# Kernel tuning notes

Measured on AMD Instinct MI355X. Metric: run time of the kernel, lower is better.

## Reference

```python
import jax, jax.numpy as jnp
import numpy as np

N = 50000        # nodes
E = 800000       # edges (pre self-loops)
H = 1            # heads
D = 64           # out_channels (incl. Lorentz time coord)
IN = 128         # in_channels
C = 1.0          # curvature c (Lorentz k)
EPS = 1e-6
NEG = 0.2        # leaky_relu negative slope


def segment_softmax(logits, seg, n):
    # numerically stable softmax over edges grouped by destination node
    m = jax.ops.segment_max(logits, seg, num_segments=n)
    m = jnp.where(jnp.isfinite(m), m, 0.0)
    e = jnp.exp(logits - m[seg])
    s = jax.ops.segment_sum(e, seg, num_segments=n)
    return e / (s[seg] + 1e-16)


def setup_inputs() -> dict:
    key = jax.random.key(0)
    k1, k2, k3, k4, k5 = jax.random.split(key, 5)
    x = jax.random.normal(k1, (N, IN), jnp.float32)
    fan = IN + H * (D - 1)
    W = jax.random.uniform(k2, (IN, H * (D - 1)), jnp.float32, -1.0, 1.0) * (6.0 / fan) ** 0.5
    b = jnp.zeros((H * (D - 1),), jnp.float32)
    att = jax.random.uniform(k3, (1, H, 2 * D), jnp.float32, -1.0, 1.0) * (6.0 / (H + 2 * D)) ** 0.5
    # random edges with no self loops (module removes them then re-adds canonical loops)
    src = jax.random.randint(k4, (E,), 0, N, jnp.int32)
    off = jax.random.randint(k5, (E,), 1, N, jnp.int32)
    dst = (src + off) % N
    edge_index = jnp.stack([src, dst], axis=0)
    return {"x": x, "W": W, "b": b, "att": att, "edge_index": edge_index}


def reference(x, W, b, att, edge_index):
    sqrt_c = C ** 0.5
    # add self loops
    loops = jnp.arange(N, dtype=edge_index.dtype)
    ei = jnp.concatenate([edge_index, jnp.stack([loops, loops])], axis=1)
    i, j = ei[0], ei[1]

    # hy_linear (plain Linear on Lorentz branch), then project to hyperboloid
    xs = (x @ W + b).reshape(N, H, D - 1)                       # space coords
    t = jnp.sqrt(jnp.sum(xs * xs, -1, keepdims=True) + C)       # time coord
    ox = jnp.concatenate([t, xs], -1)                           # (N,H,D) on manifold

    # Lorentz logmap0: d0 * (0, xs/||xs||), d0 = sqrt(c)*arccosh(x0/sqrt(c))
    nrm = jnp.sqrt(jnp.sum(xs * xs, -1, keepdims=True) + 1e-15)
    d0 = sqrt_c * jnp.arccosh(jnp.maximum(t / sqrt_c, 1.0 + EPS))
    log_x = jnp.concatenate([jnp.zeros_like(t), d0 * xs / nrm], -1)  # (N,H,D)

    x_i, x_j = log_x[i], log_x[j]        # (E2,H,D) edge gathers
    ox_i, ox_j = ox[i], ox[j]

    # attention logits
    alpha = jnp.sum(jnp.concatenate([x_i, x_j], -1) * att, -1)  # (E2,H)

    # distance-aware weighting: sqdist = c * arccosh(-<x,y>_L / c)^2
    inner = -ox_i[..., 0] * ox_j[..., 0] + jnp.sum(ox_i[..., 1:] * ox_j[..., 1:], -1)
    sqd = C * jnp.arccosh(jnp.maximum(-inner / C, 1.0 + EPS)) ** 2
    alpha = alpha * segment_softmax(sqd, i, N)

    alpha = jnp.where(alpha >= 0, alpha, NEG * alpha)           # leaky_relu
    alpha = segment_softmax(alpha, i, N)                        # (E2,H)

    out = jax.ops.segment_sum(alpha[..., None] * x_j, i, num_segments=N)  # (N,H,D)

    # proj_tan0 -> act -> proj_tan0
    out = out.at[..., 0].set(0.0)
    out = jax.nn.relu(out)
    out = out.at[..., 0].set(0.0)

    # expmap0 then projx
    usp = out[..., 1:]
    un = jnp.sqrt(jnp.sum(usp * usp, -1, keepdims=True) + 1e-15)
    sp = sqrt_c * jnp.sinh(un / sqrt_c) * usp / un
    time = jnp.sqrt(jnp.sum(sp * sp, -1, keepdims=True) + C)    # projx recomputes time
    y = jnp.concatenate([time, sp], -1)
    return y.reshape(N, H * D)
```

## Files before the change

### kernel.cpp

```cpp
#include <hip/hip_runtime.h>
#include <math.h>

#define NN 50000
#define EE 800000
#define ETOT 850000
#define INF 128
#define DD 64
#define CAP 64
#define NB_NODE ((NN + 63) / 64)
#define NB_EDGE ((ETOT + 255) / 256)
#define KCH 64
#define XP 65
#define TP 67

__device__ __forceinline__ float wsum64(float v) {
#pragma unroll
    for (int m = 1; m < 64; m <<= 1) v += __shfl_xor(v, m, 64);
    return v;
}
__device__ __forceinline__ float rlf(float v, int k) {
    return __int_as_float(__builtin_amdgcn_readlane(__float_as_int(v), k));
}

__device__ __forceinline__ float mink_full(const float* __restrict__ ox,
                                           int j, float xnv) {
    const float4* ojp = (const float4*)(ox + (size_t)(unsigned)j * DD);
    float4 oj[16];
#pragma unroll
    for (int q = 0; q < 16; ++q) oj[q] = ojp[q];
    float p0 = 0.f, p1 = 0.f, p2 = 0.f, p3 = 0.f;
#pragma unroll
    for (int q = 0; q < 16; ++q) {
        p0 = fmaf(rlf(xnv, 4 * q + 0), oj[q].x, p0);
        p1 = fmaf(rlf(xnv, 4 * q + 1), oj[q].y, p1);
        p2 = fmaf(rlf(xnv, 4 * q + 2), oj[q].z, p2);
        p3 = fmaf(rlf(xnv, 4 * q + 3), oj[q].w, p3);
    }
    return (p0 + p1 + p2 + p3) - 2.f * rlf(xnv, 0) * oj[0].x;
}

template<int NC>
__device__ __forceinline__ void gemm_q(const float* __restrict__ S,
                                       const float* __restrict__ W,
                                       int k0, int c0, int lane, float* acc) {
#pragma unroll 4
    for (int k = 0; k < KCH; ++k) {
        float xk = S[k * XP + lane];
        const float* wr = W + (size_t)(k0 + k) * 63 + c0;
#pragma unroll
        for (int c = 0; c < NC; ++c) acc[c] = fmaf(xk, wr[c], acc[c]);
    }
}

__global__ __launch_bounds__(256) void k_node_place(
    const float* __restrict__ x, const float* __restrict__ W,
    const float* __restrict__ b, const float* __restrict__ att,
    const int* __restrict__ ei0, const int* __restrict__ ei1,
    float* __restrict__ ox, float* __restrict__ ai, float2* __restrict__ snd,
    int* __restrict__ cnt, int* __restrict__ colPad)
{
    __shared__ float S[DD * TP];
    __shared__ float PP0[256], PP1[256], PP2[256];

    if (blockIdx.x >= NB_NODE) {
        int e = (blockIdx.x - NB_NODE) * 256 + threadIdx.x;
        if (e < ETOT) {
            int i, j;
            if (e < EE) { i = ei0[e]; j = ei1[e]; }
            else        { i = e - EE; j = i; }
            int pos = atomicAdd(&cnt[i], 1);
            if (pos < CAP) colPad[(size_t)i * CAP + pos] = j;
        }
        return;
    }

    const int tid  = threadIdx.x;
    const int lane = tid & 63;
    const int h    = __builtin_amdgcn_readfirstlane(tid >> 6);
    const int c0   = 16 * h;
    const int n0   = blockIdx.x * 64;
    const int n    = n0 + lane;

    float acc[16];
#pragma unroll
    for (int c = 0; c < 16; ++c) acc[c] = 0.f;

    for (int k0 = 0; k0 < INF; k0 += KCH) {
        __syncthreads();
        for (int r = 0; r < 16; ++r) {
            int e = r * 256 + tid;
            int node = e >> 6, k = e & 63;
            int gn = min(n0 + node, NN - 1);
            S[k * XP + node] = x[(size_t)gn * INF + k0 + k];
        }
        __syncthreads();
        if (h < 3) gemm_q<16>(S, W, k0, c0, lane, acc);
        else       gemm_q<15>(S, W, k0, c0, lane, acc);
    }
    const int nc = (h == 3) ? 15 : 16;

    float ssp = 0.f;
#pragma unroll
    for (int c = 0; c < 16; ++c) {
        if (c < nc) {
            acc[c] += b[c0 + c];
            ssp = fmaf(acc[c], acc[c], ssp);
        }
    }
    PP0[tid] = ssp;
    __syncthreads();
    float ss = PP0[lane] + PP0[64 + lane] + PP0[128 + lane] + PP0[192 + lane];

    float t   = sqrtf(ss + 1.0f);
    float nrm = sqrtf(ss + 1e-15f);
    float d0  = acoshf(fmaxf(t, 1.0f + 1e-6f));
    float scl = d0 / nrm;

    float aip = 0.f, ajp = 0.f;
#pragma unroll
    for (int c = 0; c < 16; ++c) {
        if (c < nc) {
            float lxv = scl * acc[c];
            aip = fmaf(lxv, att[1 + c0 + c], aip);
            ajp = fmaf(lxv, att[DD + 1 + c0 + c], ajp);
        }
    }
    PP1[tid] = aip; PP2[tid] = ajp;

#pragma unroll
    for (int c = 0; c < 16; ++c)
        if (c < nc) S[lane * TP + 1 + c0 + c] = acc[c];
    if (h == 0) S[lane * TP + 0] = t;
    __syncthreads();

    if (h == 0 && n < NN) {
        float aiv = PP1[lane] + PP1[64 + lane] + PP1[128 + lane] + PP1[192 + lane];
        float ajv = PP2[lane] + PP2[64 + lane] + PP2[128 + lane] + PP2[192 + lane];
        ai[n] = aiv;
        snd[n] = make_float2(ajv, scl);
    }

    for (int r = 0; r < 16; ++r) {
        int e = r * 256 + tid;
        int node = e >> 6, d = e & 63;
        if (n0 + node < NN)
            ox[(size_t)(n0 + node) * DD + d] = S[node * TP + d];
    }
}

__global__ __launch_bounds__(256) void k_fused(
    const int* __restrict__ cnt, const int* __restrict__ colPad,
    const float* __restrict__ ox, const float* __restrict__ ai,
    const float2* __restrict__ snd, float* __restrict__ y)
{
    const int lane = threadIdx.x & 63;
    const int wid  = threadIdx.x >> 6;
    const int n = blockIdx.x * 4 + wid;
    if (n >= NN) return;

    const int base = n * CAP;
    int deg = cnt[n];
    if (deg > CAP) deg = CAP;
    const float aii = ai[n];
    const float xnv = ox[(size_t)n * DD + lane];

    const bool act = lane < deg;
    const int  ecl = min(lane, deg - 1);
    const int  jreg = colPad[base + ecl];
    const float2 sv = snd[jreg];

    float inner = mink_full(ox, jreg, xnv);
    float arg = fmaxf(-inner, 1.0f + 1e-6f);
    float dd0 = acoshf(arg);
    float sq  = dd0 * dd0;

    float e1 = act ? expf(sq) : 0.f;
    float s1 = wsum64(e1) + 1e-16f;
    float al = (aii + sv.x) * e1 / s1;
    al = (al >= 0.f) ? al : 0.2f * al;
    float p2 = act ? expf(al) : 0.f;
    float s2 = wsum64(p2);
    float w2 = p2 / (s2 + 1e-16f) * sv.y;

    float acc = 0.f;
    int k = 0;
    for (; k + 8 <= deg; k += 8) {
        float w0 = __shfl(w2, k + 0, 64), w1 = __shfl(w2, k + 1, 64);
        float w2b = __shfl(w2, k + 2, 64), w3 = __shfl(w2, k + 3, 64);
        float w4 = __shfl(w2, k + 4, 64), w5 = __shfl(w2, k + 5, 64);
        float w6 = __shfl(w2, k + 6, 64), w7 = __shfl(w2, k + 7, 64);
        int j0 = __shfl(jreg, k + 0, 64), j1 = __shfl(jreg, k + 1, 64);
        int j2 = __shfl(jreg, k + 2, 64), j3 = __shfl(jreg, k + 3, 64);
        int j4 = __shfl(jreg, k + 4, 64), j5 = __shfl(jreg, k + 5, 64);
        int j6 = __shfl(jreg, k + 6, 64), j7 = __shfl(jreg, k + 7, 64);
        float v0 = ox[(size_t)j0 * DD + lane], v1 = ox[(size_t)j1 * DD + lane];
        float v2 = ox[(size_t)j2 * DD + lane], v3 = ox[(size_t)j3 * DD + lane];
        float v4 = ox[(size_t)j4 * DD + lane], v5 = ox[(size_t)j5 * DD + lane];
        float v6 = ox[(size_t)j6 * DD + lane], v7 = ox[(size_t)j7 * DD + lane];
        acc = fmaf(w0, v0, acc);  acc = fmaf(w1, v1, acc);
        acc = fmaf(w2b, v2, acc); acc = fmaf(w3, v3, acc);
        acc = fmaf(w4, v4, acc);  acc = fmaf(w5, v5, acc);
        acc = fmaf(w6, v6, acc);  acc = fmaf(w7, v7, acc);
    }
    for (; k < deg; ++k) {
        float w = __shfl(w2, k, 64);
        int   j = __shfl(jreg, k, 64);
        acc = fmaf(w, ox[(size_t)j * DD + lane], acc);
    }

    float usp = (lane == 0) ? 0.f : fmaxf(acc, 0.f);
    float ss = wsum64(usp * usp);
    float un = sqrtf(ss + 1e-15f);
    float sc = sinhf(un) / un;
    float sp = sc * usp;
    float time = sqrtf(sc * sc * ss + 1.0f);
    y[(size_t)n * DD + lane] = (lane == 0) ? time : sp;
}

extern "C" void kernel_launch(void* const* d_in, const int* in_sizes, int n_in,
                              void* d_out, int out_size, void* d_ws, size_t ws_size,
                              hipStream_t stream) {
    const float* x   = (const float*)d_in[0];
    const float* W   = (const float*)d_in[1];
    const float* b   = (const float*)d_in[2];
    const float* att = (const float*)d_in[3];
    const int*   ei  = (const int*)d_in[4];
    const int* ei0 = ei;
    const int* ei1 = ei + EE;
    float* out = (float*)d_out;

    float*  ws  = (float*)d_ws;
    float*  ox  = ws;
    float*  ai  = ox + (size_t)NN * DD;
    float2* snd = (float2*)(ai + NN);
    int*    cnt    = (int*)(snd + NN);
    int*    colPad = cnt + NN;

    hipMemsetAsync(cnt, 0, sizeof(int) * NN, stream);

    k_node_place<<<NB_NODE + NB_EDGE, 256, 0, stream>>>(
        x, W, b, att, ei0, ei1, ox, ai, snd, cnt, colPad);

    k_fused<<<(NN + 3) / 4, 256, 0, stream>>>(cnt, colPad, ox, ai, snd, out);
}
```

Baseline: 133.5 us.

## Process two nodes per wavefront using half-waves, with slow path for high degree

The fused edge kernel now assigns two destination nodes to each 64-lane wavefront, one per 32-lane half, and uses 32-lane reductions. Each lane computes its edge's Minkowski inner product with direct float4 loads instead of readlane broadcasts. Each lane then accumulates two output features during aggregation. If either node in the pair has more than 32 edges, the wave falls back to the original per-node path run serially for both nodes. The goal is better lane utilisation, since average degree is about 17, at the cost of divergence and a serial fallback for rare high-degree pairs.

```diff
diff --git a/kernel.cpp b/kernel.cpp
--- a/kernel.cpp
+++ b/kernel.cpp
@@ -18,6 +18,11 @@
     for (int m = 1; m < 64; m <<= 1) v += __shfl_xor(v, m, 64);
     return v;
 }
+__device__ __forceinline__ float wsum32(float v) {
+#pragma unroll
+    for (int m = 1; m < 32; m <<= 1) v += __shfl_xor(v, m, 64);
+    return v;
+}
 __device__ __forceinline__ float rlf(float v, int k) {
     return __int_as_float(__builtin_amdgcn_readlane(__float_as_int(v), k));
 }
@@ -148,6 +153,53 @@
     }
 }
 
+__device__ void slow_node(int n, const int* __restrict__ cnt,
+                          const int* __restrict__ colPad,
+                          const float* __restrict__ ox,
+                          const float* __restrict__ ai,
+                          const float2* __restrict__ snd,
+                          float* __restrict__ y, int lane)
+{
+    const int base = n * CAP;
+    int deg = cnt[n];
+    if (deg > CAP) deg = CAP;
+    const float aii = ai[n];
+    const float xnv = ox[(size_t)n * DD + lane];
+
+    const bool act = lane < deg;
+    const int  ecl = min(lane, deg - 1);
+    const int  jreg = colPad[base + ecl];
+    const float2 sv = snd[jreg];
+
+    float inner = mink_full(ox, jreg, xnv);
+    float arg = fmaxf(-inner, 1.0f + 1e-6f);
+    float dd0 = acoshf(arg);
+    float sq  = dd0 * dd0;
+
+    float e1 = act ? expf(sq) : 0.f;
+    float s1 = wsum64(e1) + 1e-16f;
+    float al = (aii + sv.x) * e1 / s1;
+    al = (al >= 0.f) ? al : 0.2f * al;
+    float p2 = act ? expf(al) : 0.f;
+    float s2 = wsum64(p2);
+    float w2 = p2 / (s2 + 1e-16f) * sv.y;
+
+    float acc = 0.f;
+    for (int k = 0; k < deg; ++k) {
+        float w = __shfl(w2, k, 64);
+        int   j = __shfl(jreg, k, 64);
+        acc = fmaf(w, ox[(size_t)j * DD + lane], acc);
+    }
+
+    float usp = (lane == 0) ? 0.f : fmaxf(acc, 0.f);
+    float ss = wsum64(usp * usp);
+    float un = sqrtf(ss + 1e-15f);
+    float sc = sinhf(un) / un;
+    float sp = sc * usp;
+    float time = sqrtf(sc * sc * ss + 1.0f);
+    y[(size_t)n * DD + lane] = (lane == 0) ? time : sp;
+}
+
 __global__ __launch_bounds__(256) void k_fused(
     const int* __restrict__ cnt, const int* __restrict__ colPad,
     const float* __restrict__ ox, const float* __restrict__ ai,
@@ -155,66 +207,88 @@
 {
     const int lane = threadIdx.x & 63;
     const int wid  = threadIdx.x >> 6;
-    const int n = blockIdx.x * 4 + wid;
-    if (n >= NN) return;
-
-    const int base = n * CAP;
+    const int pr   = blockIdx.x * 4 + wid;
+    const int nA   = pr * 2;
+    if (nA >= NN) return;
+
+    const int half = lane >> 5;
+    const int l    = lane & 31;
+    const int n    = nA + half;
+
     int deg = cnt[n];
     if (deg > CAP) deg = CAP;
-    const float aii = ai[n];
-    const float xnv = ox[(size_t)n * DD + lane];
-
-    const bool act = lane < deg;
-    const int  ecl = min(lane, deg - 1);
-    const int  jreg = colPad[base + ecl];
-    const float2 sv = snd[jreg];
-
-    float inner = mink_full(ox, jreg, xnv);
-    float arg = fmaxf(-inner, 1.0f + 1e-6f);
-    float dd0 = acoshf(arg);
-    float sq  = dd0 * dd0;
-
-    float e1 = act ? expf(sq) : 0.f;
-    float s1 = wsum64(e1) + 1e-16f;
-    float al = (aii + sv.x) * e1 / s1;
-    al = (al >= 0.f) ? al : 0.2f * al;
-    float p2 = act ? expf(al) : 0.f;
-    float s2 = wsum64(p2);
-    float w2 = p2 / (s2 + 1e-16f) * sv.y;
-
-    float acc = 0.f;
-    int k = 0;
-    for (; k + 8 <= deg; k += 8) {
-        float w0 = __shfl(w2, k + 0, 64), w1 = __shfl(w2, k + 1, 64);
-        float w2b = __shfl(w2, k + 2, 64), w3 = __shfl(w2, k + 3, 64);
-        float w4 = __shfl(w2, k + 4, 64), w5 = __shfl(w2, k + 5, 64);
-        float w6 = __shfl(w2, k + 6, 64), w7 = __shfl(w2, k + 7, 64);
-        int j0 = __shfl(jreg, k + 0, 64), j1 = __shfl(jreg, k + 1, 64);
-        int j2 = __shfl(jreg, k + 2, 64), j3 = __shfl(jreg, k + 3, 64);
-        int j4 = __shfl(jreg, k + 4, 64), j5 = __shfl(jreg, k + 5, 64);
-        int j6 = __shfl(jreg, k + 6, 64), j7 = __shfl(jreg, k + 7, 64);
-        float v0 = ox[(size_t)j0 * DD + lane], v1 = ox[(size_t)j1 * DD + lane];
-        float v2 = ox[(size_t)j2 * DD + lane], v3 = ox[(size_t)j3 * DD + lane];
-        float v4 = ox[(size_t)j4 * DD + lane], v5 = ox[(size_t)j5 * DD + lane];
-        float v6 = ox[(size_t)j6 * DD + lane], v7 = ox[(size_t)j7 * DD + lane];
-        acc = fmaf(w0, v0, acc);  acc = fmaf(w1, v1, acc);
-        acc = fmaf(w2b, v2, acc); acc = fmaf(w3, v3, acc);
-        acc = fmaf(w4, v4, acc);  acc = fmaf(w5, v5, acc);
-        acc = fmaf(w6, v6, acc);  acc = fmaf(w7, v7, acc);
-    }
-    for (; k < deg; ++k) {
-        float w = __shfl(w2, k, 64);
-        int   j = __shfl(jreg, k, 64);
-        acc = fmaf(w, ox[(size_t)j * DD + lane], acc);
-    }
-
-    float usp = (lane == 0) ? 0.f : fmaxf(acc, 0.f);
-    float ss = wsum64(usp * usp);
-    float un = sqrtf(ss + 1e-15f);
-    float sc = sinhf(un) / un;
-    float sp = sc * usp;
-    float time = sqrtf(sc * sc * ss + 1.0f);
-    y[(size_t)n * DD + lane] = (lane == 0) ? time : sp;
+
+    if (!__any(deg > 32)) {
+        const float aii = ai[n];
+        const bool act = l < deg;
+        const int  ecl = min(l, deg - 1);
+        const int  jreg = colPad[n * CAP + ecl];
+        const float2 sv = snd[jreg];
+
+        const float4* oip = (const float4*)(ox + (size_t)n * DD);
+        const float4* ojp = (const float4*)(ox + (size_t)(unsigned)jreg * DD);
+        float p0 = 0.f, p1 = 0.f, p2v = 0.f, p3 = 0.f;
+        float oi0 = 0.f, oj0 = 0.f;
+#pragma unroll
+        for (int q = 0; q < 16; ++q) {
+            float4 a = oip[q];
+            float4 bq = ojp[q];
+            if (q == 0) { oi0 = a.x; oj0 = bq.x; }
+            p0 = fmaf(a.x, bq.x, p0);
+            p1 = fmaf(a.y, bq.y, p1);
+            p2v = fmaf(a.z, bq.z, p2v);
+            p3 = fmaf(a.w, bq.w, p3);
+        }
+        float inner = (p0 + p1 + p2v + p3) - 2.f * oi0 * oj0;
+
+        float arg = fmaxf(-inner, 1.0f + 1e-6f);
+        float dd0 = acoshf(arg);
+        float sq  = dd0 * dd0;
+
+        float e1 = act ? expf(sq) : 0.f;
+        float s1 = wsum32(e1) + 1e-16f;
+        float al = (aii + sv.x) * e1 / s1;
+        al = (al >= 0.f) ? al : 0.2f * al;
+        float p2 = act ? expf(al) : 0.f;
+        float s2 = wsum32(p2);
+        float w2 = p2 / (s2 + 1e-16f) * sv.y;
+
+        float acc0 = 0.f, acc1 = 0.f;
+        const int sb = half * 32;
+        int k = 0;
+        for (; k + 4 <= deg; k += 4) {
+            float wv0 = __shfl(w2, sb + k + 0, 64), wv1 = __shfl(w2, sb + k + 1, 64);
+            float wv2 = __shfl(w2, sb + k + 2, 64), wv3 = __shfl(w2, sb + k + 3, 64);
+            int j0 = __shfl(jreg, sb + k + 0, 64), j1 = __shfl(jreg, sb + k + 1, 64);
+            int j2 = __shfl(jreg, sb + k + 2, 64), j3 = __shfl(jreg, sb + k + 3, 64);
+            float a0 = ox[(size_t)j0 * DD + l],      b0 = ox[(size_t)j0 * DD + 32 + l];
+            float a1 = ox[(size_t)j1 * DD + l],      b1 = ox[(size_t)j1 * DD + 32 + l];
+            float a2 = ox[(size_t)j2 * DD + l],      b2 = ox[(size_t)j2 * DD + 32 + l];
+            float a3 = ox[(size_t)j3 * DD + l],      b3 = ox[(size_t)j3 * DD + 32 + l];
+            acc0 = fmaf(wv0, a0, acc0); acc1 = fmaf(wv0, b0, acc1);
+            acc0 = fmaf(wv1, a1, acc0); acc1 = fmaf(wv1, b1, acc1);
+            acc0 = fmaf(wv2, a2, acc0); acc1 = fmaf(wv2, b2, acc1);
+            acc0 = fmaf(wv3, a3, acc0); acc1 = fmaf(wv3, b3, acc1);
+        }
+        for (; k < deg; ++k) {
+            float wv = __shfl(w2, sb + k, 64);
+            int   j  = __shfl(jreg, sb + k, 64);
+            acc0 = fmaf(wv, ox[(size_t)j * DD + l], acc0);
+            acc1 = fmaf(wv, ox[(size_t)j * DD + 32 + l], acc1);
+        }
+
+        float u0 = (l == 0) ? 0.f : fmaxf(acc0, 0.f);
+        float u1 = fmaxf(acc1, 0.f);
+        float ssl = wsum32(u0 * u0 + u1 * u1);
+        float un = sqrtf(ssl + 1e-15f);
+        float sc = sinhf(un) / un;
+        float time = sqrtf(sc * sc * ssl + 1.0f);
+        y[(size_t)n * DD + l]      = (l == 0) ? time : sc * u0;
+        y[(size_t)n * DD + 32 + l] = sc * u1;
+    } else {
+        slow_node(nA,     cnt, colPad, ox, ai, snd, y, lane);
+        slow_node(nA + 1, cnt, colPad, ox, ai, snd, y, lane);
+    }
 }
 
 extern "C" void kernel_launch(void* const* d_in, const int* in_sizes, int n_in,
@@ -241,5 +315,6 @@
     k_node_place<<<NB_NODE + NB_EDGE, 256, 0, stream>>>(
         x, W, b, att, ei0, ei1, ox, ai, snd, cnt, colPad);
 
-    k_fused<<<(NN + 3) / 4, 256, 0, stream>>>(cnt, colPad, ox, ai, snd, out);
-}
+    const int pairs = NN / 2;
+    k_fused<<<(pairs + 3) / 4, 256, 0, stream>>>(cnt, colPad, ox, ai, snd, out);
+}
```

Result: slower. 141.1 us (+5.7%).
